# Kernel optimization log

Hardware: AMD Instinct MI355X
Metric: run time of the kernel (lower is better)

## Reference

```python
import jax, jax.numpy as jnp
import numpy as np
from jax import lax

BIG = 1e10  # initial distance, matching torch's 1e10


def farthest_point_sample(xyz, init_farthest, npoint):
    """xyz: [B,N,3] float; init_farthest: [B] int32; returns centroids [B,npoint] int32."""
    B, N, _ = xyz.shape
    batch_idx = jnp.arange(B)

    def body(i, state):
        centroids, distance, farthest = state
        centroids = centroids.at[:, i].set(farthest)
        c = xyz[batch_idx, farthest][:, None, :]              # [B,1,3] current centroid
        dist = jnp.sum(jnp.square(xyz - c), axis=-1)          # [B,N] sq. distance
        distance = jnp.minimum(distance, dist)                # mask-update: keep min dist to any centroid
        farthest = jnp.argmax(distance, axis=-1).astype(jnp.int32)
        return centroids, distance, farthest

    centroids0 = jnp.zeros((B, npoint), jnp.int32)
    distance0 = jnp.full((B, N), BIG, xyz.dtype)
    centroids, _, _ = lax.fori_loop(0, npoint, body, (centroids0, distance0, init_farthest.astype(jnp.int32)))
    return centroids


def setup_inputs() -> dict:
    key = jax.random.key(0)
    k1, k2, k3 = jax.random.split(key, 3)
    B, N = 16, 100000
    mesh = jax.random.normal(k1, (B, N, 3), dtype=jnp.float32)
    contact_map = jax.random.uniform(k2, (B, N, 1), dtype=jnp.float32)
    init_farthest = jax.random.randint(k3, (B,), 0, N, dtype=jnp.int32)
    return {"mesh": mesh, "contact_map": contact_map, "init_farthest": init_farthest, "npoint": 1024}


def reference(mesh, contact_map, init_farthest, npoint):
    B, N, _ = mesh.shape
    batch_idx = jnp.arange(B)

    # __compute_mesh_scale: max distance from centroid, per batch
    centroid = jnp.mean(mesh, axis=1, keepdims=True)                      # [B,1,3]
    s_obj = jnp.max(jnp.sqrt(jnp.sum(jnp.square(mesh - centroid), axis=2)), axis=1)  # [B]

    # __farthest_point_sample
    centroids = farthest_point_sample(mesh, init_farthest, npoint)        # [B,npoint]

    # gather sampled points and contact values
    point_cloud = mesh[batch_idx[:, None], centroids]                     # [B,npoint,3]
    cm_sampled = contact_map[batch_idx[:, None], centroids]               # [B,npoint,1]

    # normalize by object scale (broadcast over points/coords)
    point_cloud_norm = point_cloud / s_obj[:, None, None]

    # point_cloud_norm_contact fed to the contact encoder in the original
    return jnp.concatenate([cm_sampled, point_cloud_norm], axis=2)        # [B,npoint,4]
```

## Files before the change

kernel.cpp:

```cpp
#include <hip/hip_runtime.h>
#include <cstdint>

#define NBATCH 16
#define NPOINT 1024
#define NPTS   100000
#define GPB    16
#define TPB    256
#define WPB    4
#define NSUB   16
#define STRIDE (GPB * TPB)
#define KPT    25
#define NPAIR  13

typedef unsigned long long u64;


__global__ __launch_bounds__(256) void sum_kernel(const float* __restrict__ xyz,
                                                  float* __restrict__ psum) {
    const int b   = blockIdx.x & 15;
    const int sub = blockIdx.x >> 4;
    const float* P = xyz + (size_t)b * NPTS * 3;
    float sx = 0.f, sy = 0.f, sz = 0.f;
    for (int i = sub * TPB + threadIdx.x; i < NPTS; i += NSUB * TPB) {
        sx += P[i * 3 + 0];
        sy += P[i * 3 + 1];
        sz += P[i * 3 + 2];
    }
    #pragma unroll
    for (int off = 32; off; off >>= 1) {
        sx += __shfl_xor(sx, off);
        sy += __shfl_xor(sy, off);
        sz += __shfl_xor(sz, off);
    }
    __shared__ float r[3][4];
    const int wave = threadIdx.x >> 6, lane = threadIdx.x & 63;
    if (lane == 0) { r[0][wave] = sx; r[1][wave] = sy; r[2][wave] = sz; }
    __syncthreads();
    if (threadIdx.x == 0) {
        float* o = psum + (b * NSUB + sub) * 4;
        o[0] = r[0][0] + r[0][1] + r[0][2] + r[0][3];
        o[1] = r[1][0] + r[1][1] + r[1][2] + r[1][3];
        o[2] = r[2][0] + r[2][1] + r[2][2] + r[2][3];
    }
}

__global__ __launch_bounds__(256) void max_kernel(const float* __restrict__ xyz,
                                                  const float* __restrict__ psum,
                                                  unsigned* __restrict__ pmax,
                                                  u64* __restrict__ slots) {
    if (blockIdx.x == 0) {
        slots[threadIdx.x] = 0ull;
        slots[threadIdx.x + 256] = 0ull;
    }
    const int b   = blockIdx.x & 15;
    const int sub = blockIdx.x >> 4;
    const float* P = xyz + (size_t)b * NPTS * 3;
    float sx = 0.f, sy = 0.f, sz = 0.f;
    #pragma unroll
    for (int s = 0; s < NSUB; ++s) {
        sx += psum[(b * NSUB + s) * 4 + 0];
        sy += psum[(b * NSUB + s) * 4 + 1];
        sz += psum[(b * NSUB + s) * 4 + 2];
    }
    const float mx = sx / (float)NPTS, my = sy / (float)NPTS, mz = sz / (float)NPTS;
    float best = 0.f;
    for (int i = sub * TPB + threadIdx.x; i < NPTS; i += NSUB * TPB) {
        float dx = P[i * 3 + 0] - mx;
        float dy = P[i * 3 + 1] - my;
        float dz = P[i * 3 + 2] - mz;
        best = fmaxf(best, dx * dx + dy * dy + dz * dz);
    }
    #pragma unroll
    for (int off = 32; off; off >>= 1) best = fmaxf(best, __shfl_xor(best, off));
    __shared__ float r[4];
    const int wave = threadIdx.x >> 6, lane = threadIdx.x & 63;
    if (lane == 0) r[wave] = best;
    __syncthreads();
    if (threadIdx.x == 0)
        pmax[b * NSUB + sub] = __float_as_uint(fmaxf(fmaxf(r[0], r[1]), fmaxf(r[2], r[3])));
}

__global__ __launch_bounds__(256, 1) void fps_kernel(const float* __restrict__ xyz,
                                                     const float* __restrict__ cmap,
                                                     const int* __restrict__ init_far,
                                                     const unsigned* __restrict__ pmax,
                                                     u64* __restrict__ slots,
                                                     float* __restrict__ out) {
    const int b   = blockIdx.x & 15;
    const int g   = blockIdx.x >> 4;
    const int tid = threadIdx.x;
    const int wave = tid >> 6, lane = tid & 63;
    const int tl  = g * TPB + tid;
    const float* P = xyz + (size_t)b * NPTS * 3;

    float m0 = 0.f;
    #pragma unroll
    for (int s = 0; s < NSUB; ++s) m0 = fmaxf(m0, __uint_as_float(pmax[b * NSUB + s]));
    const float sb = sqrtf(m0);

    float pxx[NPAIR], pxy[NPAIR], pyx[NPAIR], pyy[NPAIR],
          pzx[NPAIR], pzy[NPAIR], pdx[NPAIR], pdy[NPAIR];
    #pragma unroll
    for (int j = 0; j < NPAIR; ++j) {
        const int p0 = tl + (2 * j) * STRIDE;
        const int p1 = tl + (2 * j + 1) * STRIDE;
        const bool v0 = p0 < NPTS, v1 = p1 < NPTS;
        pxx[j] = v0 ? P[p0 * 3 + 0] : 0.f;  pxy[j] = v1 ? P[p1 * 3 + 0] : 0.f;
        pyx[j] = v0 ? P[p0 * 3 + 1] : 0.f;  pyy[j] = v1 ? P[p1 * 3 + 1] : 0.f;
        pzx[j] = v0 ? P[p0 * 3 + 2] : 0.f;  pzy[j] = v1 ? P[p1 * 3 + 2] : 0.f;
        pdx[j] = v0 ? 1e10f : -1.0f;        pdy[j] = v1 ? 1e10f : -1.0f;
    }

    __shared__ u64 lds_key[WPB];
    __shared__ int lds_win;
    __shared__ int curhist[NPOINT];

    int cur = init_far[b];
    float cx = P[cur * 3 + 0], cy = P[cur * 3 + 1], cz = P[cur * 3 + 2];

    for (int i = 0; i < NPOINT; ++i) {
        if (tid == 192) curhist[i] = cur;
        if (i == NPOINT - 1) break;

        float best = -1.0f;
        int bidx = 0;
        {
            #pragma clang fp contract(off)
            #pragma unroll
            for (int j = 0; j < NPAIR; ++j) {
                float dx0 = pxx[j] - cx, dx1 = pxy[j] - cx;
                float dy0 = pyx[j] - cy, dy1 = pyy[j] - cy;
                float dz0 = pzx[j] - cz, dz1 = pzy[j] - cz;
                float s0 = dx0 * dx0 + dy0 * dy0;  float s1 = dx1 * dx1 + dy1 * dy1;
                s0 = s0 + dz0 * dz0;               s1 = s1 + dz1 * dz1;
                float n0 = fminf(pdx[j], s0);      float n1 = fminf(pdy[j], s1);
                pdx[j] = n0;                       pdy[j] = n1;
                if (n0 > best) { best = n0; bidx = tl + (2 * j) * STRIDE; }
                if (n1 > best) { best = n1; bidx = tl + (2 * j + 1) * STRIDE; }
            }
        }

        const u64 want = (u64)(i + 1);
        u64 key = ((u64)__float_as_uint(best) << 22) | (u64)(0x3FFFFFu - (unsigned)bidx);
        #pragma unroll
        for (int off = 32; off; off >>= 1) {
            u64 o2 = __shfl_xor(key, off);
            key = o2 > key ? o2 : key;
        }
        if (lane == 0) lds_key[wave] = key;
        __syncthreads();

        u64* const bs = slots + ((size_t)(i & 1) * NBATCH + b) * GPB;

        if (wave == 0) {
            u64 bk = (lane < WPB) ? lds_key[lane] : 0;
            #pragma unroll
            for (int off = 1; off < WPB; off <<= 1) {
                u64 o2 = __shfl_xor(bk, off);
                bk = o2 > bk ? o2 : bk;
            }
            if (lane == 0)
                __hip_atomic_store(&bs[g], bk | (want << 54),
                                   __ATOMIC_RELAXED, __HIP_MEMORY_SCOPE_AGENT);

            u64 v = 0;
            if (lane < GPB) {
                u64* sp = &bs[lane];
                int tries = 0;
                for (;;) {
                    v = __hip_atomic_load(sp, __ATOMIC_RELAXED, __HIP_MEMORY_SCOPE_AGENT);
                    if ((v >> 54) >= want) break;
                    if (++tries > 16) __builtin_amdgcn_s_sleep(1);
                }
            }
            #pragma unroll
            for (int off = 8; off; off >>= 1) {
                u64 o2 = __shfl_xor(v, off);
                v = o2 > v ? o2 : v;
            }
            if (lane == 0)
                lds_win = (int)(0x3FFFFFu - (unsigned)(v & 0x3FFFFFu));
        }
        __syncthreads();
        cur = lds_win;
        cx = P[cur * 3 + 0];
        cy = P[cur * 3 + 1];
        cz = P[cur * 3 + 2];
    }

    __syncthreads();
    if (tid < 64) {
        const int row = g * 64 + tid;
        const int c   = curhist[row];
        const float cm = cmap[(size_t)b * NPTS + c];
        const float x = P[c * 3 + 0], y = P[c * 3 + 1], z = P[c * 3 + 2];
        float* o = out + ((size_t)b * NPOINT + row) * 4;
        o[0] = cm;
        o[1] = x / sb;
        o[2] = y / sb;
        o[3] = z / sb;
    }
}

extern "C" void kernel_launch(void* const* d_in, const int* in_sizes, int n_in,
                              void* d_out, int out_size, void* d_ws, size_t ws_size,
                              hipStream_t stream) {
    const float* mesh = (const float*)d_in[0];
    const float* cmap = (const float*)d_in[1];
    const int* init   = (const int*)d_in[2];
    float* out = (float*)d_out;

    char* ws      = (char*)d_ws;
    float* psum   = (float*)ws;
    unsigned* pmx = (unsigned*)(ws + 4096);
    u64* slots    = (u64*)(ws + 8192);

    sum_kernel<<<dim3(256), dim3(TPB), 0, stream>>>(mesh, psum);
    max_kernel<<<dim3(256), dim3(TPB), 0, stream>>>(mesh, psum, pmx, slots);
    fps_kernel<<<dim3(256), dim3(TPB), 0, stream>>>(mesh, cmap, init, pmx, slots, out);
}
```

Before: 1.994 ms.

## Publish per-wave keys globally and prefetch winner coordinates before barrier

Each wave now writes its reduced argmax key straight to a global slot array (64 slots per batch instead of 16), removing one __syncthreads and the intra-block LDS reduction per iteration. Wave 0 polls all 64 slots with one lane each, and every lane speculatively loads the coordinates of its candidate point before the cross-lane max. The winning lane then writes the index and coordinates to LDS, so the dependent global load after the barrier is gone. The cost is four times as many atomic stores and polled slots per iteration, a larger slot-zeroing pass, and up to 64 scattered coordinate loads per iteration.

```diff
diff --git a/kernel.cpp b/kernel.cpp
--- a/kernel.cpp
+++ b/kernel.cpp
@@ -7,6 +7,7 @@
 #define GPB    16
 #define TPB    256
 #define WPB    4
+#define NSLOT  (GPB * WPB)
 #define NSUB   16
 #define STRIDE (GPB * TPB)
 #define KPT    25
@@ -49,8 +50,8 @@
                                                   unsigned* __restrict__ pmax,
                                                   u64* __restrict__ slots) {
     if (blockIdx.x == 0) {
-        slots[threadIdx.x] = 0ull;
-        slots[threadIdx.x + 256] = 0ull;
+        #pragma unroll
+        for (int q = 0; q < 8; ++q) slots[threadIdx.x + q * 256] = 0ull;
     }
     const int b   = blockIdx.x & 15;
     const int sub = blockIdx.x >> 4;
@@ -111,9 +112,9 @@
         pdx[j] = v0 ? 1e10f : -1.0f;        pdy[j] = v1 ? 1e10f : -1.0f;
     }
 
-    __shared__ u64 lds_key[WPB];
-    __shared__ int lds_win;
-    __shared__ int curhist[NPOINT];
+    __shared__ int   lds_win;
+    __shared__ float lds_x, lds_y, lds_z;
+    __shared__ int   curhist[NPOINT];
 
     int cur = init_far[b];
     float cx = P[cur * 3 + 0], cy = P[cur * 3 + 1], cz = P[cur * 3 + 2];
@@ -147,24 +148,15 @@
             u64 o2 = __shfl_xor(key, off);
             key = o2 > key ? o2 : key;
         }
-        if (lane == 0) lds_key[wave] = key;
-        __syncthreads();
-
-        u64* const bs = slots + ((size_t)(i & 1) * NBATCH + b) * GPB;
+
+        u64* const bs = slots + ((size_t)(i & 1) * NBATCH + b) * NSLOT;
+        if (lane == 0)
+            __hip_atomic_store(&bs[g * WPB + wave], key | (want << 54),
+                               __ATOMIC_RELAXED, __HIP_MEMORY_SCOPE_AGENT);
 
         if (wave == 0) {
-            u64 bk = (lane < WPB) ? lds_key[lane] : 0;
-            #pragma unroll
-            for (int off = 1; off < WPB; off <<= 1) {
-                u64 o2 = __shfl_xor(bk, off);
-                bk = o2 > bk ? o2 : bk;
-            }
-            if (lane == 0)
-                __hip_atomic_store(&bs[g], bk | (want << 54),
-                                   __ATOMIC_RELAXED, __HIP_MEMORY_SCOPE_AGENT);
-
-            u64 v = 0;
-            if (lane < GPB) {
+            u64 v;
+            {
                 u64* sp = &bs[lane];
                 int tries = 0;
                 for (;;) {
@@ -173,19 +165,24 @@
                     if (++tries > 16) __builtin_amdgcn_s_sleep(1);
                 }
             }
+            const int ci = (int)(0x3FFFFFu - (unsigned)(v & 0x3FFFFFu));
+            const float gx = P[ci * 3 + 0];
+            const float gy = P[ci * 3 + 1];
+            const float gz = P[ci * 3 + 2];
+            u64 kk = v;
             #pragma unroll
-            for (int off = 8; off; off >>= 1) {
-                u64 o2 = __shfl_xor(v, off);
-                v = o2 > v ? o2 : v;
-            }
-            if (lane == 0)
-                lds_win = (int)(0x3FFFFFu - (unsigned)(v & 0x3FFFFFu));
+            for (int off = 32; off; off >>= 1) {
+                u64 o2 = __shfl_xor(kk, off);
+                kk = o2 > kk ? o2 : kk;
+            }
+            if (v == kk) {
+                lds_win = ci;
+                lds_x = gx; lds_y = gy; lds_z = gz;
+            }
         }
         __syncthreads();
         cur = lds_win;
-        cx = P[cur * 3 + 0];
-        cy = P[cur * 3 + 1];
-        cz = P[cur * 3 + 2];
+        cx = lds_x; cy = lds_y; cz = lds_z;
     }
 
     __syncthreads();
```

Result: slower. 4.246 ms (+113.0%).
